# Performance work log

Measured on AMD Instinct MI355X. Metric: run time of the kernel, lower is better.

The kernel has to match this reference:

```python
import jax, jax.numpy as jnp
import numpy as np

GAMMA = 0.6
EPS = 1e-10
T = 20
ALPHA = 2.0
BETA = 1.5
LAM = 2.0
ETA = 10.0
PLACEHOLDER = -1
ENABLE_BONUS = False

B, K, V = 64, 8, 50257


def _nan_to(x, val):
    # torch.nan_to_num(nan=val) replaces only NaN, keeps +-inf
    return jnp.where(jnp.isnan(x), jnp.asarray(val, x.dtype), x)


def _costeer(llm, base, steer):
    # llm/base/steer: [B, V]
    llm_log = jax.nn.log_softmax(_nan_to(llm, -100.0), axis=-1)
    base_log = jax.nn.log_softmax(_nan_to(base, -100.0), axis=-1)
    steer_log = jax.nn.log_softmax(_nan_to(steer, -100.0), axis=-1)
    delta = steer_log - base_log
    delta = jnp.where(jnp.isnan(delta), jnp.zeros((), delta.dtype), delta)

    def body(t, carry):
        q_sum, log_p, prev = carry
        q_sum = q_sum + ALPHA * (log_p - llm_log) + BETA * delta
        t_f = t.astype(llm_log.dtype)
        denom = t_f * LAM + 1.0 / ETA
        lp = (t_f * LAM * llm_log + q_sum + prev / ETA) / denom
        lp = jax.nn.log_softmax(lp, axis=-1)
        return (q_sum, lp, lp)

    q0 = jnp.zeros_like(llm_log)
    _, log_p, _ = jax.lax.fori_loop(1, T + 1, body, (q0, llm_log, llm_log))
    return log_p


def setup_inputs() -> dict:
    key = jax.random.key(0)
    k1, k2, k3, k4, k5, k6 = jax.random.split(key, 6)
    target_logits = jax.random.normal(k1, (B * K, V), dtype=jnp.float32)
    base_logits = jax.random.normal(k2, (B * K, V), dtype=jnp.float32)
    steer_logits = jax.random.normal(k3, (B * K, V), dtype=jnp.float32)
    draft_token_ids = jax.random.randint(k4, (B, K), 0, V, dtype=jnp.int32)
    num_draft_tokens = jax.random.randint(k5, (B,), 1, K + 1, dtype=jnp.int32)
    bonus_token_ids = jax.random.randint(k6, (B,), 0, V, dtype=jnp.int32)
    return {
        "target_logits": target_logits,
        "base_logits": base_logits,
        "steer_logits": steer_logits,
        "draft_token_ids": draft_token_ids,
        "num_draft_tokens": num_draft_tokens,
        "bonus_token_ids": bonus_token_ids,
    }


def reference(target_logits, base_logits, steer_logits, draft_token_ids,
              num_draft_tokens, bonus_token_ids):
    tl = target_logits.reshape(B, K, V)
    bl = base_logits.reshape(B, K, V)
    sl = steer_logits.reshape(B, K, V)

    target_probs = jax.nn.softmax(tl, axis=-1)
    base_probs = jax.nn.softmax(bl, axis=-1)

    idx = draft_token_ids[..., None]  # [B, K, 1]
    p_llm = jnp.take_along_axis(target_probs, idx, axis=-1)[..., 0]  # [B, K]
    p_base = jnp.take_along_axis(base_probs, idx, axis=-1)[..., 0]

    pos = jnp.arange(K, dtype=jnp.int32)[None, :]           # [1, K]
    valid = pos < num_draft_tokens[:, None]                  # [B, K]
    accept = (p_llm > GAMMA * (p_base + EPS)) & valid
    prefix = jnp.cumprod(accept.astype(jnp.int32), axis=1)   # 1 until first reject
    cnt = prefix.sum(axis=1).astype(jnp.int32)               # accepted count [B]
    rejected = cnt < num_draft_tokens                        # [B]

    # gather the (first-rejected) row per request; clamp for fully-accepted reqs
    rp = jnp.minimum(cnt, K - 1)[:, None, None]              # [B,1,1]
    llm_r = jnp.take_along_axis(tl, rp, axis=1)[:, 0]        # [B, V]
    base_r = jnp.take_along_axis(bl, rp, axis=1)[:, 0]
    steer_r = jnp.take_along_axis(sl, rp, axis=1)[:, 0]

    fused = _costeer(llm_r, base_r, steer_r)                 # [B, V]
    recovered = jnp.argmax(fused, axis=-1).astype(jnp.int32)  # [B]

    ph = jnp.full((B, K), PLACEHOLDER, dtype=jnp.int32)
    out_main = jnp.where(pos < cnt[:, None], draft_token_ids,
                         jnp.where((pos == cnt[:, None]) & rejected[:, None],
                                   recovered[:, None], ph))  # [B, K]

    if ENABLE_BONUS:
        bonus_col = jnp.where(~rejected, bonus_token_ids,
                              jnp.full((B,), PLACEHOLDER, jnp.int32))[:, None]
    else:
        bonus_col = jnp.full((B, 1), PLACEHOLDER, dtype=jnp.int32)
    output_token_ids = jnp.concatenate([out_main, bonus_col], axis=1)  # [B, K+1]

    return output_token_ids, cnt, fused
```

## Files before the change

### kernel.cpp

```cpp
#include <hip/hip_runtime.h>
#include <cstdint>
#include <cstddef>

#define VDIM 50257
#define BNUM 64
#define KNUM 8
#define TITER 20
#define TPB2 512
#define EPT ((VDIM + TPB2 - 1) / TPB2)


__device__ __forceinline__ void onl(float& m, float& s, float x) {
    if (x > m) { s = s * __expf(m - x) + 1.0f; m = x; }
    else       { s += __expf(x - m); }
}

__device__ __forceinline__ void comb(float& m, float& s, float mo, float so) {
    float mn = fmaxf(m, mo);
    s = s * __expf(m - mn) + so * __expf(mo - mn);
    m = mn;
}

template <int NWAVES>
__device__ __forceinline__ void blockReduceMS(float& m, float& s, float* shm, int tid) {
    int lane = tid & 63;
    int wid  = tid >> 6;
    #pragma unroll
    for (int off = 32; off > 0; off >>= 1) {
        float mo = __shfl_down(m, off);
        float so = __shfl_down(s, off);
        comb(m, s, mo, so);
    }
    if (lane == 0) { shm[2 * wid] = m; shm[2 * wid + 1] = s; }
    __syncthreads();
    if (tid == 0) {
        float M = shm[0], S = shm[1];
        #pragma unroll
        for (int w = 1; w < NWAVES; w++) comb(M, S, shm[2 * w], shm[2 * w + 1]);
        shm[0] = M; shm[1] = S;
    }
    __syncthreads();
    m = shm[0];
    s = shm[1];
    __syncthreads();
}

template <int NWAVES>
__device__ __forceinline__ void blockReduceArgmax(float& v, int& idx, float* shmf, int* shmi, int tid) {
    int lane = tid & 63;
    int wid  = tid >> 6;
    #pragma unroll
    for (int off = 32; off > 0; off >>= 1) {
        float vo = __shfl_down(v, off);
        int   io = __shfl_down(idx, off);
        if (vo > v || (vo == v && io < idx)) { v = vo; idx = io; }
    }
    if (lane == 0) { shmf[wid] = v; shmi[wid] = idx; }
    __syncthreads();
    if (tid == 0) {
        #pragma unroll
        for (int w = 1; w < NWAVES; w++) {
            if (shmf[w] > v || (shmf[w] == v && shmi[w] < idx)) { v = shmf[w]; idx = shmi[w]; }
        }
        shmf[0] = v; shmi[0] = idx;
    }
    __syncthreads();
    v = shmf[0];
    idx = shmi[0];
    __syncthreads();
}


__global__ __launch_bounds__(256) void k_stats(
        const float* __restrict__ tgt, const float* __restrict__ bse,
        const int* __restrict__ draft, const int* __restrict__ ndraft,
        float* __restrict__ p_out ) {
    int id    = blockIdx.x;
    int which = id >> 9;
    int r     = id & 511;
    int k     = r & (KNUM - 1);
    int b     = r >> 3;
    if (k >= ndraft[b]) return;

    const float* row = (which ? bse : tgt) + (size_t)r * VDIM;
    int tid = threadIdx.x;

    float m = -3.0e38f, s = 0.0f;

    int mis  = (int)(((uintptr_t)row & 15) >> 2);
    int head = (4 - mis) & 3;
    if (tid < head) onl(m, s, row[tid]);

    const float4* v4 = (const float4*)(row + head);
    int n4 = (VDIM - head) >> 2;
    for (int g = tid; g < n4; g += 256) {
        float4 x = v4[g];
        onl(m, s, x.x); onl(m, s, x.y); onl(m, s, x.z); onl(m, s, x.w);
    }
    int done = head + (n4 << 2);
    int j = done + tid;
    if (j < VDIM) onl(m, s, row[j]);

    __shared__ float shm[16];
    blockReduceMS<4>(m, s, shm, tid);

    if (tid == 0) {
        float lse = m + __logf(s);
        int tok = draft[r];
        p_out[which * 512 + r] = __expf(row[tok] - lse);
    }
}


__global__ __launch_bounds__(TPB2, 2) void k_main(
        const float* __restrict__ tgt, const float* __restrict__ bse,
        const float* __restrict__ str,
        const int* __restrict__ draft, const int* __restrict__ ndraft,
        const float* __restrict__ p_llm, const float* __restrict__ p_base,
        float* __restrict__ out_tok,
        float* __restrict__ out_cnt,
        float* __restrict__ out_fused  ) {
    int b   = blockIdx.x;
    int tid = threadIdx.x;

    __shared__ int   sh_rp, sh_cnt, sh_rej;
    __shared__ float shm[16];
    __shared__ int   shmi[8];

    if (tid == 0) {
        int nd  = ndraft[b];
        int cnt = 0;
        bool chain = true;
        for (int k = 0; k < KNUM; k++) {
            float pl = p_llm[b * KNUM + k];
            float pb = p_base[b * KNUM + k];
            bool acc = (k < nd) && (pl > 0.6f * (pb + 1e-10f));
            chain = chain && acc;
            if (chain) cnt++;
        }
        int rej = (cnt < nd) ? 1 : 0;
        int rp  = cnt < (KNUM - 1) ? cnt : (KNUM - 1);
        for (int k = 0; k < KNUM; k++) {
            int tokv = (k < cnt) ? draft[b * KNUM + k] : -1;
            out_tok[b * (KNUM + 1) + k] = (float)tokv;
        }
        out_tok[b * (KNUM + 1) + KNUM] = -1.0f;
        out_cnt[b] = (float)cnt;
        sh_rp = rp; sh_cnt = cnt; sh_rej = rej;
    }
    __syncthreads();

    int rp = sh_rp;
    size_t roff = (size_t)(b * KNUM + rp) * VDIM;
    const float* tl = tgt + roff;
    const float* bl = bse + roff;
    const float* sl = str + roff;

    float dd = 0.0f, ee = 0.0f, aa = 1.0f, bb = 0.0f;
    #pragma unroll
    for (int t = 1; t <= TITER; t++) {
        dd += 2.0f * (aa - 1.0f);
        ee += 2.0f * bb + 1.5f;
        float tf = (float)t;
        float denom = tf * 2.0f + 0.1f;
        float an = (tf * 2.0f + dd + aa * 0.1f) / denom;
        float bn = (ee + bb * 0.1f) / denom;
        aa = an; bb = bn;
    }

    float Y[EPT];
    float m = -3.0e38f, s = 0.0f;
    float bv = -3.0e38f;
    int   bi = 0x7fffffff;
    #pragma unroll
    for (int i = 0; i < EPT; i++) {
        int j = tid + i * TPB2;
        float y = 0.0f;
        if (j < VDIM) {
            y = aa * tl[j] + bb * (sl[j] - bl[j]);
            onl(m, s, y);
            if (y > bv) { bv = y; bi = j; }
        }
        Y[i] = y;
    }
    blockReduceMS<8>(m, s, shm, tid);
    float Z = m + __logf(s);
    blockReduceArgmax<8>(bv, bi, shm, shmi, tid);

    #pragma unroll
    for (int i = 0; i < EPT; i++) {
        int j = tid + i * TPB2;
        if (j < VDIM) out_fused[(size_t)b * VDIM + j] = Y[i] - Z;
    }

    if (tid == 0 && sh_rej) {
        out_tok[b * (KNUM + 1) + sh_cnt] = (float)bi;
    }
}


extern "C" void kernel_launch(void* const* d_in, const int* in_sizes, int n_in,
                              void* d_out, int out_size, void* d_ws, size_t ws_size,
                              hipStream_t stream) {
    const float* tgt   = (const float*)d_in[0];
    const float* bse   = (const float*)d_in[1];
    const float* str   = (const float*)d_in[2];
    const int*   draft = (const int*)d_in[3];
    const int*   nd    = (const int*)d_in[4];

    float* out       = (float*)d_out;
    float* out_tok   = out;
    float* out_cnt   = out + BNUM * (KNUM + 1);
    float* out_fused = out + BNUM * (KNUM + 1) + BNUM;

    float* p_llm  = (float*)d_ws;
    float* p_base = p_llm + BNUM * KNUM;

    hipLaunchKernelGGL(k_stats, dim3(1024), dim3(256), 0, stream,
                       tgt, bse, draft, nd, p_llm);
    hipLaunchKernelGGL(k_main, dim3(BNUM), dim3(TPB2), 0, stream,
                       tgt, bse, str, draft, nd, p_llm, p_llm + BNUM * KNUM,
                       out_tok, out_cnt, out_fused);
}
```

Measured before the change: 320.4 us.

## Fuse stats and main into one cooperative kernel with split-row reductions

```diff
diff --git a/kernel.cpp b/kernel.cpp
--- a/kernel.cpp
+++ b/kernel.cpp
@@ -1,13 +1,19 @@
 #include <hip/hip_runtime.h>
+#include <hip/hip_cooperative_groups.h>
 #include <cstdint>
 #include <cstddef>
+
+namespace cg = cooperative_groups;
 
 #define VDIM 50257
 #define BNUM 64
 #define KNUM 8
 #define TITER 20
-#define TPB2 512
-#define EPT ((VDIM + TPB2 - 1) / TPB2)
+#define NBLK 512
+#define TPB 256
+#define SEGN 8
+#define SEGLEN 6283
+#define EPT3 25
 
 
 __device__ __forceinline__ void onl(float& m, float& s, float x) {
@@ -21,7 +27,6 @@
     m = mn;
 }
 
-template <int NWAVES>
 __device__ __forceinline__ void blockReduceMS(float& m, float& s, float* shm, int tid) {
     int lane = tid & 63;
     int wid  = tid >> 6;
@@ -36,7 +41,7 @@
     if (tid == 0) {
         float M = shm[0], S = shm[1];
         #pragma unroll
-        for (int w = 1; w < NWAVES; w++) comb(M, S, shm[2 * w], shm[2 * w + 1]);
+        for (int w = 1; w < 4; w++) comb(M, S, shm[2 * w], shm[2 * w + 1]);
         shm[0] = M; shm[1] = S;
     }
     __syncthreads();
@@ -45,7 +50,6 @@
     __syncthreads();
 }
 
-template <int NWAVES>
 __device__ __forceinline__ void blockReduceArgmax(float& v, int& idx, float* shmf, int* shmi, int tid) {
     int lane = tid & 63;
     int wid  = tid >> 6;
@@ -59,7 +63,7 @@
     __syncthreads();
     if (tid == 0) {
         #pragma unroll
-        for (int w = 1; w < NWAVES; w++) {
+        for (int w = 1; w < 4; w++) {
             if (shmf[w] > v || (shmf[w] == v && shmi[w] < idx)) { v = shmf[w]; idx = shmi[w]; }
         }
         shmf[0] = v; shmi[0] = idx;
@@ -70,87 +74,95 @@
     __syncthreads();
 }
 
-
-__global__ __launch_bounds__(256) void k_stats(
-        const float* __restrict__ tgt, const float* __restrict__ bse,
-        const int* __restrict__ draft, const int* __restrict__ ndraft,
-        float* __restrict__ p_out ) {
-    int id    = blockIdx.x;
-    int which = id >> 9;
-    int r     = id & 511;
-    int k     = r & (KNUM - 1);
-    int b     = r >> 3;
-    if (k >= ndraft[b]) return;
-
-    const float* row = (which ? bse : tgt) + (size_t)r * VDIM;
-    int tid = threadIdx.x;
-
-    float m = -3.0e38f, s = 0.0f;
-
+__device__ __forceinline__ void row_stats(const float* __restrict__ row, int tid,
+                                          float& m, float& s) {
+    m = -3.0e38f; s = 0.0f;
     int mis  = (int)(((uintptr_t)row & 15) >> 2);
     int head = (4 - mis) & 3;
     if (tid < head) onl(m, s, row[tid]);
-
     const float4* v4 = (const float4*)(row + head);
     int n4 = (VDIM - head) >> 2;
-    for (int g = tid; g < n4; g += 256) {
+    for (int g = tid; g < n4; g += TPB) {
         float4 x = v4[g];
         onl(m, s, x.x); onl(m, s, x.y); onl(m, s, x.z); onl(m, s, x.w);
     }
     int done = head + (n4 << 2);
     int j = done + tid;
     if (j < VDIM) onl(m, s, row[j]);
-
-    __shared__ float shm[16];
-    blockReduceMS<4>(m, s, shm, tid);
-
-    if (tid == 0) {
-        float lse = m + __logf(s);
-        int tok = draft[r];
-        p_out[which * 512 + r] = __expf(row[tok] - lse);
-    }
-}
-
-
-__global__ __launch_bounds__(TPB2, 2) void k_main(
+}
+
+
+__global__ __launch_bounds__(TPB) void k_coop(
         const float* __restrict__ tgt, const float* __restrict__ bse,
         const float* __restrict__ str,
         const int* __restrict__ draft, const int* __restrict__ ndraft,
-        const float* __restrict__ p_llm, const float* __restrict__ p_base,
-        float* __restrict__ out_tok,
-        float* __restrict__ out_cnt,
-        float* __restrict__ out_fused  ) {
-    int b   = blockIdx.x;
-    int tid = threadIdx.x;
-
-    __shared__ int   sh_rp, sh_cnt, sh_rej;
+        float* __restrict__ out_tok, float* __restrict__ out_cnt,
+        float* __restrict__ out_fused,
+        float* __restrict__ wsf, int* __restrict__ wsi) {
+    cg::grid_group grid = cg::this_grid();
+    int blk = blockIdx.x, tid = threadIdx.x;
+
     __shared__ float shm[16];
     __shared__ int   shmi[8];
-
-    if (tid == 0) {
-        int nd  = ndraft[b];
+    __shared__ float sh_Z;
+    __shared__ int   sh_gi;
+
+    float* p_all = wsf;
+    float* pm    = wsf + 1024;
+    float* ps    = wsf + 1536;
+    float* pv    = wsf + 2048;
+    int* rp_arr  = wsi;
+    int* cnt_arr = wsi + 64;
+    int* rej_arr = wsi + 128;
+    int* pi      = wsi + 192;
+
+    {
+        int r = blk;
+        int b1 = r >> 3, k1 = r & (KNUM - 1);
+        if (k1 < ndraft[b1]) {
+            #pragma unroll
+            for (int which = 0; which < 2; which++) {
+                const float* row = (which ? bse : tgt) + (size_t)r * VDIM;
+                float m, s;
+                row_stats(row, tid, m, s);
+                blockReduceMS(m, s, shm, tid);
+                if (tid == 0) {
+                    float lse = m + __logf(s);
+                    p_all[which * 512 + r] = __expf(row[draft[r]] - lse);
+                }
+                __syncthreads();
+            }
+        }
+    }
+    __threadfence();
+    grid.sync();
+
+    if (blk == 0 && tid < BNUM) {
+        int b = tid;
+        int nd = ndraft[b];
         int cnt = 0;
         bool chain = true;
         for (int k = 0; k < KNUM; k++) {
-            float pl = p_llm[b * KNUM + k];
-            float pb = p_base[b * KNUM + k];
+            float pl = p_all[b * KNUM + k];
+            float pb = p_all[512 + b * KNUM + k];
             bool acc = (k < nd) && (pl > 0.6f * (pb + 1e-10f));
             chain = chain && acc;
             if (chain) cnt++;
         }
         int rej = (cnt < nd) ? 1 : 0;
         int rp  = cnt < (KNUM - 1) ? cnt : (KNUM - 1);
-        for (int k = 0; k < KNUM; k++) {
-            int tokv = (k < cnt) ? draft[b * KNUM + k] : -1;
-            out_tok[b * (KNUM + 1) + k] = (float)tokv;
-        }
+        for (int k = 0; k < KNUM; k++)
+            out_tok[b * (KNUM + 1) + k] = (k < cnt) ? (float)draft[b * KNUM + k] : -1.0f;
         out_tok[b * (KNUM + 1) + KNUM] = -1.0f;
         out_cnt[b] = (float)cnt;
-        sh_rp = rp; sh_cnt = cnt; sh_rej = rej;
-    }
-    __syncthreads();
-
-    int rp = sh_rp;
+        rp_arr[b] = rp; cnt_arr[b] = cnt; rej_arr[b] = rej;
+    }
+    __threadfence();
+    grid.sync();
+
+    int b   = blk >> 3;
+    int seg = blk & (SEGN - 1);
+    int rp  = rp_arr[b];
     size_t roff = (size_t)(b * KNUM + rp) * VDIM;
     const float* tl = tgt + roff;
     const float* bl = bse + roff;
@@ -168,33 +180,54 @@
         aa = an; bb = bn;
     }
 
-    float Y[EPT];
+    int start = seg * SEGLEN;
+    int len   = VDIM - start; if (len > SEGLEN) len = SEGLEN;
+
+    float Y[EPT3];
     float m = -3.0e38f, s = 0.0f;
     float bv = -3.0e38f;
     int   bi = 0x7fffffff;
     #pragma unroll
-    for (int i = 0; i < EPT; i++) {
-        int j = tid + i * TPB2;
+    for (int i = 0; i < EPT3; i++) {
+        int j = tid + i * TPB;
         float y = 0.0f;
-        if (j < VDIM) {
-            y = aa * tl[j] + bb * (sl[j] - bl[j]);
+        if (j < len) {
+            int g = start + j;
+            y = aa * tl[g] + bb * (sl[g] - bl[g]);
             onl(m, s, y);
-            if (y > bv) { bv = y; bi = j; }
+            if (y > bv) { bv = y; bi = g; }
         }
         Y[i] = y;
     }
-    blockReduceMS<8>(m, s, shm, tid);
-    float Z = m + __logf(s);
-    blockReduceArgmax<8>(bv, bi, shm, shmi, tid);
-
-    #pragma unroll
-    for (int i = 0; i < EPT; i++) {
-        int j = tid + i * TPB2;
-        if (j < VDIM) out_fused[(size_t)b * VDIM + j] = Y[i] - Z;
-    }
-
-    if (tid == 0 && sh_rej) {
-        out_tok[b * (KNUM + 1) + sh_cnt] = (float)bi;
+    blockReduceMS(m, s, shm, tid);
+    blockReduceArgmax(bv, bi, shm, shmi, tid);
+    if (tid == 0) { pm[blk] = m; ps[blk] = s; pv[blk] = bv; pi[blk] = bi; }
+    __threadfence();
+    grid.sync();
+
+    if (tid == 0) {
+        float M = -3.0e38f, S = 0.0f;
+        float gv = -3.0e38f;
+        int   gi = 0x7fffffff;
+        #pragma unroll
+        for (int sg = 0; sg < SEGN; sg++) {
+            int idx = b * SEGN + sg;
+            comb(M, S, pm[idx], ps[idx]);
+            float v = pv[idx]; int ii = pi[idx];
+            if (v > gv || (v == gv && ii < gi)) { gv = v; gi = ii; }
+        }
+        sh_Z  = M + __logf(S);
+        sh_gi = gi;
+    }
+    __syncthreads();
+    float Z = sh_Z;
+    #pragma unroll
+    for (int i = 0; i < EPT3; i++) {
+        int j = tid + i * TPB;
+        if (j < len) out_fused[(size_t)b * VDIM + start + j] = Y[i] - Z;
+    }
+    if (seg == 0 && tid == 0 && rej_arr[b]) {
+        out_tok[b * (KNUM + 1) + cnt_arr[b]] = (float)sh_gi;
     }
 }
 
@@ -213,12 +246,12 @@
     float* out_cnt   = out + BNUM * (KNUM + 1);
     float* out_fused = out + BNUM * (KNUM + 1) + BNUM;
 
-    float* p_llm  = (float*)d_ws;
-    float* p_base = p_llm + BNUM * KNUM;
-
-    hipLaunchKernelGGL(k_stats, dim3(1024), dim3(256), 0, stream,
-                       tgt, bse, draft, nd, p_llm);
-    hipLaunchKernelGGL(k_main, dim3(BNUM), dim3(TPB2), 0, stream,
-                       tgt, bse, str, draft, nd, p_llm, p_llm + BNUM * KNUM,
-                       out_tok, out_cnt, out_fused);
-}
+    float* wsf = (float*)d_ws;
+    int*   wsi = (int*)(wsf + 2560);
+
+    void* args[] = { (void*)&tgt, (void*)&bse, (void*)&str, (void*)&draft,
+                     (void*)&nd, (void*)&out_tok, (void*)&out_cnt,
+                     (void*)&out_fused, (void*)&wsf, (void*)&wsi };
+    hipLaunchCooperativeKernel((const void*)k_coop, dim3(NBLK), dim3(TPB),
+                               args, 0, stream);
+}
```

Measured after the change: 612.2 us. +91.1%, slower.

## Split row reductions across segments and parallelize fused log-softmax over many blocks

Applied to the files above, without the earlier changes.

```diff
diff --git a/kernel.cpp b/kernel.cpp
--- a/kernel.cpp
+++ b/kernel.cpp
@@ -6,13 +6,20 @@
 #define BNUM 64
 #define KNUM 8
 #define TITER 20
-#define TPB2 512
-#define EPT ((VDIM + TPB2 - 1) / TPB2)
-
-
-__device__ __forceinline__ void onl(float& m, float& s, float x) {
-    if (x > m) { s = s * __expf(m - x) + 1.0f; m = x; }
-    else       { s += __expf(x - m); }
+
+#define SEGA   12564
+#define NSEGA  4
+#define SEGF   1572
+#define NSEGF  32
+#define EPTF   7
+
+__device__ __forceinline__ void upd(float& m, float& s, float x) {
+    float d = m - x;
+    float e = __expf(-fabsf(d));
+    float t1 = (d >= 0.0f) ? 1.0f : e;
+    float t2 = (d >= 0.0f) ? e : 1.0f;
+    s = fmaf(s, t1, t2);
+    m = fmaxf(m, x);
 }
 
 __device__ __forceinline__ void comb(float& m, float& s, float mo, float so) {
@@ -21,10 +28,8 @@
     m = mn;
 }
 
-template <int NWAVES>
 __device__ __forceinline__ void blockReduceMS(float& m, float& s, float* shm, int tid) {
-    int lane = tid & 63;
-    int wid  = tid >> 6;
+    int lane = tid & 63, wid = tid >> 6;
     #pragma unroll
     for (int off = 32; off > 0; off >>= 1) {
         float mo = __shfl_down(m, off);
@@ -36,19 +41,16 @@
     if (tid == 0) {
         float M = shm[0], S = shm[1];
         #pragma unroll
-        for (int w = 1; w < NWAVES; w++) comb(M, S, shm[2 * w], shm[2 * w + 1]);
+        for (int w = 1; w < 4; w++) comb(M, S, shm[2 * w], shm[2 * w + 1]);
         shm[0] = M; shm[1] = S;
     }
     __syncthreads();
-    m = shm[0];
-    s = shm[1];
-    __syncthreads();
-}
-
-template <int NWAVES>
+    m = shm[0]; s = shm[1];
+    __syncthreads();
+}
+
 __device__ __forceinline__ void blockReduceArgmax(float& v, int& idx, float* shmf, int* shmi, int tid) {
-    int lane = tid & 63;
-    int wid  = tid >> 6;
+    int lane = tid & 63, wid = tid >> 6;
     #pragma unroll
     for (int off = 32; off > 0; off >>= 1) {
         float vo = __shfl_down(v, off);
@@ -59,105 +61,220 @@
     __syncthreads();
     if (tid == 0) {
         #pragma unroll
-        for (int w = 1; w < NWAVES; w++) {
+        for (int w = 1; w < 4; w++)
             if (shmf[w] > v || (shmf[w] == v && shmi[w] < idx)) { v = shmf[w]; idx = shmi[w]; }
-        }
         shmf[0] = v; shmi[0] = idx;
     }
     __syncthreads();
-    v = shmf[0];
-    idx = shmi[0];
-    __syncthreads();
-}
-
+    v = shmf[0]; idx = shmi[0];
+    __syncthreads();
+}
 
 __global__ __launch_bounds__(256) void k_stats(
         const float* __restrict__ tgt, const float* __restrict__ bse,
-        const int* __restrict__ draft, const int* __restrict__ ndraft,
-        float* __restrict__ p_out ) {
-    int id    = blockIdx.x;
-    int which = id >> 9;
-    int r     = id & 511;
-    int k     = r & (KNUM - 1);
-    int b     = r >> 3;
-    if (k >= ndraft[b]) return;
+        const int* __restrict__ ndraft,
+        float* __restrict__ pm_a, float* __restrict__ ps_a) {
+    int bid  = blockIdx.x;
+    int task = bid >> 2, seg = bid & 3;
+    int which = task >> 9, r = task & 511;
+    if ((r & 7) >= ndraft[r >> 3]) return;
 
     const float* row = (which ? bse : tgt) + (size_t)r * VDIM;
+    int start = seg * SEGA;
+    int len = VDIM - start; if (len > SEGA) len = SEGA;
+    const float* p = row + start;
     int tid = threadIdx.x;
 
-    float m = -3.0e38f, s = 0.0f;
-
-    int mis  = (int)(((uintptr_t)row & 15) >> 2);
+    float m0 = -3.0e38f, m1 = -3.0e38f, m2 = -3.0e38f, m3 = -3.0e38f;
+    float s0 = 0.f, s1 = 0.f, s2 = 0.f, s3 = 0.f;
+
+    int mis  = (int)(((uintptr_t)p & 15) >> 2);
     int head = (4 - mis) & 3;
-    if (tid < head) onl(m, s, row[tid]);
-
-    const float4* v4 = (const float4*)(row + head);
-    int n4 = (VDIM - head) >> 2;
+    if (tid < head) upd(m0, s0, p[tid]);
+    const float4* v4 = (const float4*)(p + head);
+    int n4 = (len - head) >> 2;
     for (int g = tid; g < n4; g += 256) {
         float4 x = v4[g];
-        onl(m, s, x.x); onl(m, s, x.y); onl(m, s, x.z); onl(m, s, x.w);
-    }
-    int done = head + (n4 << 2);
-    int j = done + tid;
-    if (j < VDIM) onl(m, s, row[j]);
+        upd(m0, s0, x.x); upd(m1, s1, x.y); upd(m2, s2, x.z); upd(m3, s3, x.w);
+    }
+    int j = head + (n4 << 2) + tid;
+    if (j < len) upd(m0, s0, p[j]);
+
+    comb(m0, s0, m1, s1);
+    comb(m2, s2, m3, s3);
+    comb(m0, s0, m2, s2);
 
     __shared__ float shm[16];
-    blockReduceMS<4>(m, s, shm, tid);
-
-    if (tid == 0) {
-        float lse = m + __logf(s);
-        int tok = draft[r];
-        p_out[which * 512 + r] = __expf(row[tok] - lse);
-    }
-}
-
-
-__global__ __launch_bounds__(TPB2, 2) void k_main(
-        const float* __restrict__ tgt, const float* __restrict__ bse,
-        const float* __restrict__ str,
+    blockReduceMS(m0, s0, shm, tid);
+    if (tid == 0) { pm_a[bid] = m0; ps_a[bid] = s0; }
+}
+
+__global__ __launch_bounds__(1024) void k_accept(
+        const float* __restrict__ tgt, const float* __restrict__ bse,
         const int* __restrict__ draft, const int* __restrict__ ndraft,
-        const float* __restrict__ p_llm, const float* __restrict__ p_base,
-        float* __restrict__ out_tok,
-        float* __restrict__ out_cnt,
-        float* __restrict__ out_fused  ) {
-    int b   = blockIdx.x;
-    int tid = threadIdx.x;
-
-    __shared__ int   sh_rp, sh_cnt, sh_rej;
-    __shared__ float shm[16];
-    __shared__ int   shmi[8];
-
-    if (tid == 0) {
-        int nd  = ndraft[b];
-        int cnt = 0;
-        bool chain = true;
-        for (int k = 0; k < KNUM; k++) {
-            float pl = p_llm[b * KNUM + k];
-            float pb = p_base[b * KNUM + k];
-            bool acc = (k < nd) && (pl > 0.6f * (pb + 1e-10f));
+        const float* __restrict__ pm_a, const float* __restrict__ ps_a,
+        float* __restrict__ out_tok, float* __restrict__ out_cnt,
+        int* __restrict__ rci ) {
+    __shared__ float shp[1024];
+    int t = threadIdx.x;
+    int which = t >> 9, r = t & 511;
+    int b = r >> 3, k = r & 7;
+
+    float pval = 0.0f;
+    if (k < ndraft[b]) {
+        float M = -3.0e38f, S = 0.0f;
+        #pragma unroll
+        for (int sg = 0; sg < NSEGA; sg++) comb(M, S, pm_a[t * 4 + sg], ps_a[t * 4 + sg]);
+        float lse = M + __logf(S);
+        const float* row = (which ? bse : tgt) + (size_t)r * VDIM;
+        pval = __expf(row[draft[r]] - lse);
+    }
+    shp[t] = pval;
+    __syncthreads();
+
+    if (t < BNUM) {
+        int nd = ndraft[t];
+        int cnt = 0; bool chain = true;
+        #pragma unroll
+        for (int kk = 0; kk < KNUM; kk++) {
+            float pl = shp[t * KNUM + kk];
+            float pb = shp[512 + t * KNUM + kk];
+            bool acc = (kk < nd) && (pl > 0.6f * (pb + 1e-10f));
             chain = chain && acc;
             if (chain) cnt++;
         }
         int rej = (cnt < nd) ? 1 : 0;
         int rp  = cnt < (KNUM - 1) ? cnt : (KNUM - 1);
-        for (int k = 0; k < KNUM; k++) {
-            int tokv = (k < cnt) ? draft[b * KNUM + k] : -1;
-            out_tok[b * (KNUM + 1) + k] = (float)tokv;
-        }
-        out_tok[b * (KNUM + 1) + KNUM] = -1.0f;
-        out_cnt[b] = (float)cnt;
-        sh_rp = rp; sh_cnt = cnt; sh_rej = rej;
-    }
-    __syncthreads();
-
-    int rp = sh_rp;
+        #pragma unroll
+        for (int kk = 0; kk < KNUM; kk++)
+            out_tok[t * (KNUM + 1) + kk] = (kk < cnt) ? (float)draft[t * KNUM + kk] : -1.0f;
+        out_tok[t * (KNUM + 1) + KNUM] = -1.0f;
+        out_cnt[t] = (float)cnt;
+        rci[t] = rp; rci[64 + t] = cnt; rci[128 + t] = rej;
+    }
+}
+
+__global__ __launch_bounds__(256) void k_fpart(
+        const float* __restrict__ tgt, const float* __restrict__ bse,
+        const float* __restrict__ str, const int* __restrict__ rci,
+        float aa, float bb,
+        float* __restrict__ pmf, float* __restrict__ psf,
+        float* __restrict__ pvf, int* __restrict__ pif) {
+    int blk = blockIdx.x;
+    int b = blk >> 5, seg = blk & (NSEGF - 1);
+    int tid = threadIdx.x;
+    int rp = rci[b];
     size_t roff = (size_t)(b * KNUM + rp) * VDIM;
     const float* tl = tgt + roff;
     const float* bl = bse + roff;
     const float* sl = str + roff;
 
+    int start = seg * SEGF;
+    int len = VDIM - start; if (len > SEGF) len = SEGF;
+
+    float m = -3.0e38f, s = 0.0f, bv = -3.0e38f;
+    int bi = 0x7fffffff;
+    #pragma unroll
+    for (int i = 0; i < EPTF; i++) {
+        int j = tid + i * 256;
+        if (j < len) {
+            int g = start + j;
+            float y = fmaf(aa, tl[g], bb * (sl[g] - bl[g]));
+            upd(m, s, y);
+            if (y > bv) { bv = y; bi = g; }
+        }
+    }
+    __shared__ float shm[16];
+    __shared__ int   shmi[8];
+    blockReduceMS(m, s, shm, tid);
+    blockReduceArgmax(bv, bi, shm, shmi, tid);
+    if (tid == 0) { pmf[blk] = m; psf[blk] = s; pvf[blk] = bv; pif[blk] = bi; }
+}
+
+__global__ __launch_bounds__(256) void k_final(
+        const float* __restrict__ tgt, const float* __restrict__ bse,
+        const float* __restrict__ str, const int* __restrict__ rci,
+        const float* __restrict__ pmf, const float* __restrict__ psf,
+        const float* __restrict__ pvf, const int* __restrict__ pif,
+        float aa, float bb,
+        float* __restrict__ out_tok, float* __restrict__ out_fused) {
+    int blk = blockIdx.x;
+    int b = blk >> 5, seg = blk & (NSEGF - 1);
+    int tid = threadIdx.x;
+
+    __shared__ float shZ;
+    __shared__ int   shG;
+
+    if (tid < 64) {
+        float M = -3.0e38f, S = 0.0f, V = -3.0e38f;
+        int I = 0x7fffffff;
+        if (tid < NSEGF) {
+            int idx = b * NSEGF + tid;
+            M = pmf[idx]; S = psf[idx]; V = pvf[idx]; I = pif[idx];
+        }
+        #pragma unroll
+        for (int off = 32; off > 0; off >>= 1) {
+            float Mo = __shfl_down(M, off);
+            float So = __shfl_down(S, off);
+            float Vo = __shfl_down(V, off);
+            int   Io = __shfl_down(I, off);
+            comb(M, S, Mo, So);
+            if (Vo > V || (Vo == V && Io < I)) { V = Vo; I = Io; }
+        }
+        if (tid == 0) { shZ = M + __logf(S); shG = I; }
+    }
+    __syncthreads();
+    float Z = shZ;
+
+    int rp = rci[b];
+    size_t roff = (size_t)(b * KNUM + rp) * VDIM;
+    const float* tl = tgt + roff;
+    const float* bl = bse + roff;
+    const float* sl = str + roff;
+
+    int start = seg * SEGF;
+    int len = VDIM - start; if (len > SEGF) len = SEGF;
+    float* dst = out_fused + (size_t)b * VDIM + start;
+    #pragma unroll
+    for (int i = 0; i < EPTF; i++) {
+        int j = tid + i * 256;
+        if (j < len) {
+            int g = start + j;
+            float y = fmaf(aa, tl[g], bb * (sl[g] - bl[g]));
+            dst[j] = y - Z;
+        }
+    }
+    if (seg == 0 && tid == 0 && rci[128 + b]) {
+        out_tok[b * (KNUM + 1) + rci[64 + b]] = (float)shG;
+    }
+}
+
+
+extern "C" void kernel_launch(void* const* d_in, const int* in_sizes, int n_in,
+                              void* d_out, int out_size, void* d_ws, size_t ws_size,
+                              hipStream_t stream) {
+    const float* tgt   = (const float*)d_in[0];
+    const float* bse   = (const float*)d_in[1];
+    const float* str   = (const float*)d_in[2];
+    const int*   draft = (const int*)d_in[3];
+    const int*   nd    = (const int*)d_in[4];
+
+    float* out       = (float*)d_out;
+    float* out_tok   = out;
+    float* out_cnt   = out + BNUM * (KNUM + 1);
+    float* out_fused = out + BNUM * (KNUM + 1) + BNUM;
+
+    float* wsf  = (float*)d_ws;
+    float* pm_a = wsf;
+    float* ps_a = wsf + 4096;
+    float* pmf  = wsf + 8192;
+    float* psf  = wsf + 10240;
+    float* pvf  = wsf + 12288;
+    int*   wsi  = (int*)(wsf + 14336);
+    int*   rci  = wsi;
+    int*   pif  = wsi + 192;
+
     float dd = 0.0f, ee = 0.0f, aa = 1.0f, bb = 0.0f;
-    #pragma unroll
     for (int t = 1; t <= TITER; t++) {
         dd += 2.0f * (aa - 1.0f);
         ee += 2.0f * bb + 1.5f;
@@ -168,57 +285,13 @@
         aa = an; bb = bn;
     }
 
-    float Y[EPT];
-    float m = -3.0e38f, s = 0.0f;
-    float bv = -3.0e38f;
-    int   bi = 0x7fffffff;
-    #pragma unroll
-    for (int i = 0; i < EPT; i++) {
-        int j = tid + i * TPB2;
-        float y = 0.0f;
-        if (j < VDIM) {
-            y = aa * tl[j] + bb * (sl[j] - bl[j]);
-            onl(m, s, y);
-            if (y > bv) { bv = y; bi = j; }
-        }
-        Y[i] = y;
-    }
-    blockReduceMS<8>(m, s, shm, tid);
-    float Z = m + __logf(s);
-    blockReduceArgmax<8>(bv, bi, shm, shmi, tid);
-
-    #pragma unroll
-    for (int i = 0; i < EPT; i++) {
-        int j = tid + i * TPB2;
-        if (j < VDIM) out_fused[(size_t)b * VDIM + j] = Y[i] - Z;
-    }
-
-    if (tid == 0 && sh_rej) {
-        out_tok[b * (KNUM + 1) + sh_cnt] = (float)bi;
-    }
-}
-
-
-extern "C" void kernel_launch(void* const* d_in, const int* in_sizes, int n_in,
-                              void* d_out, int out_size, void* d_ws, size_t ws_size,
-                              hipStream_t stream) {
-    const float* tgt   = (const float*)d_in[0];
-    const float* bse   = (const float*)d_in[1];
-    const float* str   = (const float*)d_in[2];
-    const int*   draft = (const int*)d_in[3];
-    const int*   nd    = (const int*)d_in[4];
-
-    float* out       = (float*)d_out;
-    float* out_tok   = out;
-    float* out_cnt   = out + BNUM * (KNUM + 1);
-    float* out_fused = out + BNUM * (KNUM + 1) + BNUM;
-
-    float* p_llm  = (float*)d_ws;
-    float* p_base = p_llm + BNUM * KNUM;
-
-    hipLaunchKernelGGL(k_stats, dim3(1024), dim3(256), 0, stream,
-                       tgt, bse, draft, nd, p_llm);
-    hipLaunchKernelGGL(k_main, dim3(BNUM), dim3(TPB2), 0, stream,
-                       tgt, bse, str, draft, nd, p_llm, p_llm + BNUM * KNUM,
-                       out_tok, out_cnt, out_fused);
-}
+    hipLaunchKernelGGL(k_stats, dim3(1024 * NSEGA), dim3(256), 0, stream,
+                       tgt, bse, nd, pm_a, ps_a);
+    hipLaunchKernelGGL(k_accept, dim3(1), dim3(1024), 0, stream,
+                       tgt, bse, draft, nd, pm_a, ps_a, out_tok, out_cnt, rci);
+    hipLaunchKernelGGL(k_fpart, dim3(BNUM * NSEGF), dim3(256), 0, stream,
+                       tgt, bse, str, rci, aa, bb, pmf, psf, pvf, pif);
+    hipLaunchKernelGGL(k_final, dim3(BNUM * NSEGF), dim3(256), 0, stream,
+                       tgt, bse, str, rci, pmf, psf, pvf, pif, aa, bb,
+                       out_tok, out_fused);
+}
```

After: 273.8 us. 14.6% less time.
